# Performance work log

Measured on AMD Instinct MI355X. Metric: run time of the kernel, lower is better.

The kernel has to match this reference:

```python
import jax, jax.numpy as jnp
import numpy as np

# AlphaFold-style Invariant Point Attention (the StructureModule's core op)
N, SD, PD, C, H, PQ, PV = 768, 384, 128, 16, 12, 4, 8
W_C = (2.0 / (9.0 * PQ)) ** 0.5   # point-distance weight
W_L = (1.0 / 3.0) ** 0.5          # logit balancing weight
INV_SQRT_C = C ** -0.5


def setup_inputs() -> dict:
    key = jax.random.key(0)
    ks = jax.random.split(key, 11)
    single_rep = jax.random.normal(ks[0], (N, SD), jnp.float32)
    pair_rep = jax.random.normal(ks[1], (N, N, PD), jnp.float32)
    # random rigid frames: proper orthonormal rotations via QR + translations
    M = jax.random.normal(ks[2], (N, 3, 3), jnp.float32)
    frames_R, _ = jnp.linalg.qr(M)
    frames_t = jax.random.normal(ks[3], (N, 3), jnp.float32) * 10.0
    s = 0.02
    W_qkv = jax.random.normal(ks[4], (SD, 3 * H * C), jnp.float32) * s
    W_b = jax.random.normal(ks[5], (PD, H), jnp.float32) * s
    W_qkp = jax.random.normal(ks[6], (SD, 2 * H * PQ * 3), jnp.float32) * s
    W_vp = jax.random.normal(ks[7], (SD, H * PV * 3), jnp.float32) * s
    gamma = jnp.zeros((H,), jnp.float32)
    W_out = jax.random.normal(ks[8], (H * (PD + C + 3 * PV + PV), SD), jnp.float32) * s
    b_out = jnp.zeros((SD,), jnp.float32)
    return dict(single_rep=single_rep, pair_rep=pair_rep, frames_R=frames_R,
                frames_t=frames_t, W_qkv=W_qkv, W_b=W_b, W_qkp=W_qkp,
                W_vp=W_vp, gamma=gamma, W_out=W_out, b_out=b_out)


def reference(single_rep, pair_rep, frames_R, frames_t,
              W_qkv, W_b, W_qkp, W_vp, gamma, W_out, b_out):
    n = single_rep.shape[0]
    # scalar q/k/v: [n, C, H] (module views as (proj_dim, n_heads))
    q, k, v = [x.reshape(n, C, H) for x in jnp.split(single_rep @ W_qkv, 3, axis=-1)]
    b = jnp.einsum('ijd,dh->ijh', pair_rep, W_b)             # pair bias [n,n,H]
    qp, kp = [x.reshape(n, PQ, 3, H) for x in jnp.split(single_rep @ W_qkp, 2, axis=-1)]
    vp = (single_rep @ W_vp).reshape(n, PV, 3, H)

    def to_global(p):  # apply frame T_i = (R_i, t_i) to local points
        return jnp.einsum('nxy,npyh->npxh', frames_R, p) + frames_t[:, None, :, None]

    qg, kg, vg = to_global(qp), to_global(kp), to_global(vp)

    # squared distances sum_p ||T_i q_p - T_j k_p||^2 without [n,n,PQ,3,H] temp
    sq = jnp.sum(qg * qg, axis=(1, 2))                       # [n,H]
    sk = jnp.sum(kg * kg, axis=(1, 2))                       # [n,H]
    cross = jnp.einsum('ipxh,jpxh->ijh', qg, kg)             # [n,n,H]
    dist2 = sq[:, None, :] + sk[None, :, :] - 2.0 * cross

    head_w = jax.nn.softplus(gamma)                          # per-head gamma
    logits = W_L * (INV_SQRT_C * jnp.einsum('ich,jch->ijh', q, k)
                    + b - 0.5 * W_C * head_w * dist2)
    attn = jax.nn.softmax(logits, axis=1)                    # softmax over j

    o_pair = jnp.einsum('ijh,ijd->ihd', attn, pair_rep)      # [n,H,PD]
    o = jnp.einsum('ijh,jch->ihc', attn, v)                  # [n,H,C]
    og = jnp.einsum('ijh,jpxh->ipxh', attn, vg)              # [n,PV,3,H]
    # back to local frame: R_i^T (og - t_i)
    ol = jnp.einsum('nyx,npyh->npxh', frames_R, og - frames_t[:, None, :, None])
    onorm = jnp.sqrt(jnp.sum(ol * ol, axis=2) + 1e-8)        # [n,PV,H]

    feats = jnp.concatenate([
        o_pair.reshape(n, -1),
        o.reshape(n, -1),
        jnp.moveaxis(ol, -1, 1).reshape(n, -1),
        jnp.moveaxis(onorm, -1, 1).reshape(n, -1)], axis=-1)  # [n, H*(PD+C+3PV+PV)]
    return feats @ W_out + b_out
```

## Files before the change

### kernel.cpp

```cpp
#include <hip/hip_runtime.h>
#include <hip/hip_bf16.h>

typedef float v4f __attribute__((ext_vector_type(4)));
typedef short bf8 __attribute__((ext_vector_type(8)));
typedef unsigned short u16;

constexpr float W_C_ = 0.23570226039551584f;
constexpr float W_L_ = 0.5773502691896258f;

__device__ __forceinline__ u16 f2bf(float f) {
  unsigned u = __float_as_uint(f);
  return (u16)((u + 0x7FFFu + ((u >> 16) & 1u)) >> 16);
}
__device__ __forceinline__ float bf2f(u16 h) {
  return __uint_as_float(((unsigned)h) << 16);
}
__device__ __forceinline__ float dot4(v4f a, v4f b) {
  return a.x * b.x + a.y * b.y + a.z * b.z + a.w * b.w;
}

__global__ __launch_bounds__(256) void convert_bf(const float* __restrict__ src,
                                                  u16* __restrict__ dst, int n8) {
  int idx = blockIdx.x * 256 + threadIdx.x;
  if (idx < n8) {
    v4f a = ((const v4f*)src)[idx * 2];
    v4f b = ((const v4f*)src)[idx * 2 + 1];
    bf8 o;
    o[0] = (short)f2bf(a.x); o[1] = (short)f2bf(a.y);
    o[2] = (short)f2bf(a.z); o[3] = (short)f2bf(a.w);
    o[4] = (short)f2bf(b.x); o[5] = (short)f2bf(b.y);
    o[6] = (short)f2bf(b.z); o[7] = (short)f2bf(b.w);
    ((bf8*)dst)[idx] = o;
  }
}

__global__ __launch_bounds__(256) void wfrag_k(const float* __restrict__ W,
                                               u16* __restrict__ frag,
                                               int K, int N) {
  __shared__ float Ws[32 * 384];
  const int ks = blockIdx.x, k0 = ks * 32, t = threadIdx.x;
  const int NTfull = (N + 15) >> 4;
  for (int n0 = 0; n0 < N; n0 += 384) {
    int PN = N - n0; if (PN > 384) PN = 384;
    __syncthreads();
    for (int idx = t; idx < 32 * PN; idx += 256) {
      int r = idx / PN, c = idx - r * PN;
      Ws[r * PN + c] = W[(size_t)(k0 + r) * N + n0 + c];
    }
    __syncthreads();
    int NTp = (PN + 15) >> 4;
    for (int c = t; c < NTp * 64; c += 256) {
      int nt = c >> 6, l = c & 63;
      int col = nt * 16 + (l & 15);
      bf8 o;
#pragma unroll
      for (int e = 0; e < 8; e++) {
        int rr = (l >> 4) * 8 + e;
        float f = (col < PN) ? Ws[rr * PN + col] : 0.f;
        o[e] = (short)f2bf(f);
      }
      ((bf8*)frag)[((size_t)ks * NTfull + (n0 >> 4) + nt) * 64 + l] = o;
    }
  }
}

__global__ __launch_bounds__(256) void gemm_f32(
    const float* __restrict__ A, const float* __restrict__ B,
    float* __restrict__ C, int M, int N, int K) {
  __shared__ float AsT[32][68];
  __shared__ float Bs[32][36];
  const int bi = blockIdx.y * 64, bj = blockIdx.x * 32;
  const int t = threadIdx.x, ty = t >> 4, tx = t & 15;
  v4f acc0 = {0.f, 0.f, 0.f, 0.f}, acc1 = {0.f, 0.f, 0.f, 0.f};
  for (int k0 = 0; k0 < K; k0 += 32) {
#pragma unroll
    for (int q = 0; q < 2; q++) {
      int idx = t + 256 * q;
      int row = idx >> 3, c4 = idx & 7;
      v4f av = *(const v4f*)(A + (size_t)(bi + row) * K + k0 + c4 * 4);
      AsT[c4 * 4 + 0][row] = av.x;
      AsT[c4 * 4 + 1][row] = av.y;
      AsT[c4 * 4 + 2][row] = av.z;
      AsT[c4 * 4 + 3][row] = av.w;
    }
    {
      int r = t >> 3, c4 = t & 7;
      *(v4f*)&Bs[r][c4 * 4] = *(const v4f*)(B + (size_t)(k0 + r) * N + bj + c4 * 4);
    }
    __syncthreads();
#pragma unroll
    for (int kk = 0; kk < 32; kk++) {
      v4f a = *(const v4f*)&AsT[kk][ty * 4];
      float b0 = Bs[kk][tx * 2], b1 = Bs[kk][tx * 2 + 1];
      acc0 += a * b0;
      acc1 += a * b1;
    }
    __syncthreads();
  }
#pragma unroll
  for (int e = 0; e < 4; e++) {
    int row = bi + ty * 4 + e;
    C[(size_t)row * N + bj + tx * 2] = acc0[e];
    C[(size_t)row * N + bj + tx * 2 + 1] = acc1[e];
  }
}

__global__ __launch_bounds__(256) void mfma_gemm(
    const u16* __restrict__ Abf, const u16* __restrict__ Bfrag,
    const float* __restrict__ bias, float* __restrict__ C,
    int M, int N, int K, int ldc) {
  __shared__ u16 As[64 * 32];
  const int t = threadIdx.x, w = t >> 6, l = t & 63;
  const int bi = blockIdx.y * 64, nt0 = blockIdx.x * 2;
  const int NT = N >> 4, KS = K >> 5;
  v4f acc0 = {0.f, 0.f, 0.f, 0.f}, acc1 = {0.f, 0.f, 0.f, 0.f};
  const int srow = t >> 2, sc = t & 3;
  const int wslot = (sc ^ (srow & 3)) * 8;
  const bf8* Bf = (const bf8*)Bfrag;

  bf8 areg = *(const bf8*)(Abf + (size_t)(bi + srow) * K + sc * 8);
  bf8 b0 = Bf[(size_t)(0 * NT + nt0) * 64 + l];
  bf8 b1 = Bf[(size_t)(0 * NT + nt0 + 1) * 64 + l];
  const int rdoff = (w * 16 + (l & 15)) * 32 + (((l >> 4) ^ (l & 3)) * 8);
  for (int ks = 0; ks < KS; ks++) {
    *(bf8*)&As[srow * 32 + wslot] = areg;
    bf8 an, bn0, bn1;
    if (ks + 1 < KS) {
      an = *(const bf8*)(Abf + (size_t)(bi + srow) * K + (ks + 1) * 32 + sc * 8);
      bn0 = Bf[(size_t)((ks + 1) * NT + nt0) * 64 + l];
      bn1 = Bf[(size_t)((ks + 1) * NT + nt0 + 1) * 64 + l];
    }
    __syncthreads();
    bf8 af = *(const bf8*)&As[rdoff];
    acc0 = __builtin_amdgcn_mfma_f32_16x16x32_bf16(af, b0, acc0, 0, 0, 0);
    acc1 = __builtin_amdgcn_mfma_f32_16x16x32_bf16(af, b1, acc1, 0, 0, 0);
    __syncthreads();
    areg = an; b0 = bn0; b1 = bn1;
  }
  int col0 = nt0 * 16 + (l & 15), col1 = col0 + 16;
  float bb0 = bias ? bias[col0] : 0.f;
  float bb1 = bias ? bias[col1] : 0.f;
#pragma unroll
  for (int r = 0; r < 4; r++) {
    int row = bi + w * 16 + (l >> 4) * 4 + r;
    C[(size_t)row * ldc + col0] = acc0[r] + bb0;
    C[(size_t)row * ldc + col1] = acc1[r] + bb1;
  }
}

__global__ __launch_bounds__(256) void prep_kernel(
    const float* __restrict__ projQKV, const float* __restrict__ projQKP,
    const float* __restrict__ projVP, const float* __restrict__ fR,
    const float* __restrict__ ft,
    float* __restrict__ qbuf, float* __restrict__ v2buf,
    float* __restrict__ qgbuf, float* __restrict__ sqbuf,
    float* __restrict__ kTT) {
  const int n = blockIdx.x, t = threadIdx.x;
  __shared__ float R[9], tt[3];
  __shared__ float qgL[144], kgL[144];
  if (t < 9) R[t] = fR[n * 9 + t];
  if (t < 3) tt[t] = ft[n * 3 + t];
  __syncthreads();
  const float* rQKV = projQKV + (size_t)n * 576;
  const float* rQKP = projQKP + (size_t)n * 288;
  const float* rVP = projVP + (size_t)n * 288;
  if (t < 192) {
    int h = t >> 4, c = t & 15;
    qbuf[(size_t)n * 192 + t] = rQKV[c * 12 + h];
    kTT[(size_t)(h * 29 + c) * 768 + n] = rQKV[192 + c * 12 + h];
    v2buf[(size_t)n * 480 + h * 40 + c] = rQKV[384 + c * 12 + h];
  }
  if (t < 144) {
    int e = t / 12, h = t % 12;
    int p = e / 3, x = e % 3;
    float aq = tt[x], ak = tt[x];
#pragma unroll
    for (int y = 0; y < 3; y++) {
      float r = R[x * 3 + y];
      aq += r * rQKP[p * 36 + y * 12 + h];
      ak += r * rQKP[144 + p * 36 + y * 12 + h];
    }
    qgL[h * 12 + e] = aq;
    kgL[h * 12 + e] = ak;
    qgbuf[(size_t)n * 144 + h * 12 + e] = aq;
    kTT[(size_t)(h * 29 + 16 + e) * 768 + n] = ak;
  }
  for (int idx = t; idx < 288; idx += 256) {
    int e = idx / 12, h = idx % 12;
    int p = e / 3, x = e % 3;
    float a = tt[x];
#pragma unroll
    for (int y = 0; y < 3; y++) a += R[x * 3 + y] * rVP[p * 36 + y * 12 + h];
    v2buf[(size_t)n * 480 + h * 40 + 16 + e] = a;
  }
  __syncthreads();
  if (t < 12) {
    float s = 0.f;
#pragma unroll
    for (int e = 0; e < 12; e++) { float v = qgL[t * 12 + e]; s += v * v; }
    sqbuf[n * 12 + t] = s;
  } else if (t < 24) {
    int h = t - 12;
    float s = 0.f;
#pragma unroll
    for (int e = 0; e < 12; e++) { float v = kgL[h * 12 + e]; s += v * v; }
    kTT[(size_t)(h * 29 + 28) * 768 + n] = s;
  }
}

__global__ __launch_bounds__(256) void bias_mfma(
    const float* __restrict__ pair, const u16* __restrict__ WbFrag,
    u16* __restrict__ bbuf) {
  const int jt = blockIdx.x, i = blockIdx.y;
  const int t = threadIdx.x, w = t >> 6, l = t & 63;
  __shared__ u16 pS[64 * 128];
  bf8 bf[4];
  const bf8* Wf = (const bf8*)WbFrag;
#pragma unroll
  for (int ks = 0; ks < 4; ks++) bf[ks] = Wf[ks * 64 + l];
  const float* pg = pair + ((size_t)i * 768 + jt * 64) * 128;
#pragma unroll
  for (int it = 0; it < 4; it++) {
    int idx = t + 256 * it;
    int j = idx >> 4, c = idx & 15;
    v4f x0 = *(const v4f*)(pg + j * 128 + c * 8);
    v4f x1 = *(const v4f*)(pg + j * 128 + c * 8 + 4);
    bf8 pk;
    pk[0] = (short)f2bf(x0.x); pk[1] = (short)f2bf(x0.y);
    pk[2] = (short)f2bf(x0.z); pk[3] = (short)f2bf(x0.w);
    pk[4] = (short)f2bf(x1.x); pk[5] = (short)f2bf(x1.y);
    pk[6] = (short)f2bf(x1.z); pk[7] = (short)f2bf(x1.w);
    *(bf8*)&pS[j * 128 + ((c ^ (j & 15)) * 8)] = pk;
  }
  __syncthreads();
  v4f acc = {0.f, 0.f, 0.f, 0.f};
#pragma unroll
  for (int ks = 0; ks < 4; ks++) {
    int slot = (ks * 4 + (l >> 4)) ^ (l & 15);
    bf8 af = *(const bf8*)&pS[(w * 16 + (l & 15)) * 128 + slot * 8];
    acc = __builtin_amdgcn_mfma_f32_16x16x32_bf16(af, bf[ks], acc, 0, 0, 0);
  }
  int h = l & 15;
  if (h < 12) {
    int jbase = jt * 64 + w * 16 + (l >> 4) * 4;
    u16* dst = bbuf + ((size_t)i * 12 + h) * 768 + jbase;
#pragma unroll
    for (int r = 0; r < 4; r++) dst[r] = f2bf(acc[r]);
  }
}

__global__ __launch_bounds__(256) void qk_softmax(
    const float* __restrict__ qbuf, const float* __restrict__ qgbuf,
    const float* __restrict__ sqbuf, const float* __restrict__ kTT,
    const u16* __restrict__ bbuf, const float* __restrict__ gamma,
    u16* __restrict__ attn) {
  const int h = blockIdx.x, i = blockIdx.y, t = threadIdx.x;
  __shared__ float red[8];
  float q[16], qg[12];
  const float* qb = qbuf + (size_t)i * 192 + h * 16;
  const float* qgb = qgbuf + (size_t)i * 144 + h * 12;
#pragma unroll
  for (int c = 0; c < 16; c++) q[c] = qb[c];
#pragma unroll
  for (int e = 0; e < 12; e++) qg[e] = qgb[e];
  float sq = sqbuf[i * 12 + h];
  float g = gamma[h];
  float hw = fmaxf(g, 0.f) + log1pf(expf(-fabsf(g)));
  const float* kb = kTT + (size_t)h * 29 * 768;
  const u16* brow = bbuf + ((size_t)i * 12 + h) * 768;
  float lg[3];
#pragma unroll
  for (int s = 0; s < 3; s++) {
    int j = t + 256 * s;
    float qk = 0.f;
#pragma unroll
    for (int c = 0; c < 16; c++) qk += q[c] * kb[c * 768 + j];
    float cr = 0.f;
#pragma unroll
    for (int e = 0; e < 12; e++) cr += qg[e] * kb[(16 + e) * 768 + j];
    float sk = kb[28 * 768 + j];
    float b = bf2f(brow[j]);
    float d2 = sq + sk - 2.f * cr;
    lg[s] = W_L_ * (0.25f * qk + b - 0.5f * W_C_ * hw * d2);
  }
  float m = fmaxf(fmaxf(lg[0], lg[1]), lg[2]);
#pragma unroll
  for (int o = 32; o >= 1; o >>= 1) m = fmaxf(m, __shfl_xor(m, o));
  if ((t & 63) == 0) red[t >> 6] = m;
  __syncthreads();
  m = fmaxf(fmaxf(red[0], red[1]), fmaxf(red[2], red[3]));
  float p0 = __expf(lg[0] - m), p1 = __expf(lg[1] - m), p2 = __expf(lg[2] - m);
  float ss = p0 + p1 + p2;
#pragma unroll
  for (int o = 32; o >= 1; o >>= 1) ss += __shfl_xor(ss, o);
  if ((t & 63) == 0) red[4 + (t >> 6)] = ss;
  __syncthreads();
  float inv = 1.f / (red[4] + red[5] + red[6] + red[7]);
  u16* arow = attn + ((size_t)i * 12 + h) * 768;
  arow[t] = f2bf(p0 * inv);
  arow[t + 256] = f2bf(p1 * inv);
  arow[t + 512] = f2bf(p2 * inv);
}

__global__ __launch_bounds__(256) void opair_k(
    const float* __restrict__ pair, const u16* __restrict__ attn,
    u16* __restrict__ feats_bf) {
  const int i = blockIdx.x, t = threadIdx.x;
  const int w = t >> 6, l = t & 63;
  const int dq = l & 31, hh = l >> 5;
  __shared__ float pairL[64][132];
  __shared__ float ALf[12][68];
  v4f acc[6];
#pragma unroll
  for (int k = 0; k < 6; k++) acc[k] = (v4f){0.f, 0.f, 0.f, 0.f};

  v4f pr[8];
  bf8 areg;
  {
    const float* pg = pair + ((size_t)i * 768) * 128;
#pragma unroll
    for (int it = 0; it < 8; it++) {
      int idx = t + 256 * it;
      pr[it] = *(const v4f*)(pg + (idx >> 5) * 128 + (idx & 31) * 4);
    }
    if (t < 96)
      areg = *(const bf8*)(attn + ((size_t)i * 12 + (t >> 3)) * 768 + (t & 7) * 8);
  }
  for (int jt = 0; jt < 12; jt++) {
#pragma unroll
    for (int it = 0; it < 8; it++) {
      int idx = t + 256 * it;
      *(v4f*)&pairL[idx >> 5][(idx & 31) * 4] = pr[it];
    }
    if (t < 96) {
      int hA = t >> 3, c = t & 7;
#pragma unroll
      for (int e = 0; e < 8; e++) ALf[hA][c * 8 + e] = bf2f((u16)areg[e]);
    }
    if (jt < 11) {
      const float* pg = pair + ((size_t)i * 768 + (jt + 1) * 64) * 128;
#pragma unroll
      for (int it = 0; it < 8; it++) {
        int idx = t + 256 * it;
        pr[it] = *(const v4f*)(pg + (idx >> 5) * 128 + (idx & 31) * 4);
      }
      if (t < 96)
        areg = *(const bf8*)(attn + ((size_t)i * 12 + (t >> 3)) * 768 +
                             (jt + 1) * 64 + (t & 7) * 8);
    }
    __syncthreads();
#pragma unroll
    for (int jj16 = 0; jj16 < 16; jj16++) {
      int jj = w * 16 + jj16;
      v4f pv = *(const v4f*)&pairL[jj][dq * 4];
      float a0 = ALf[hh * 6 + 0][jj];
      float a1 = ALf[hh * 6 + 1][jj];
      float a2 = ALf[hh * 6 + 2][jj];
      float a3 = ALf[hh * 6 + 3][jj];
      float a4 = ALf[hh * 6 + 4][jj];
      float a5 = ALf[hh * 6 + 5][jj];
      acc[0] += pv * a0; acc[1] += pv * a1; acc[2] += pv * a2;
      acc[3] += pv * a3; acc[4] += pv * a4; acc[5] += pv * a5;
    }
    __syncthreads();
  }
  float* red = &pairL[0][0];
#pragma unroll
  for (int k = 0; k < 6; k++)
    *(v4f*)&red[((w * 12 + hh * 6 + k) << 7) + dq * 4] = acc[k];
  __syncthreads();
  const size_t fb = (size_t)i * 2112;
#pragma unroll
  for (int s = 0; s < 6; s++) {
    int o = t + 256 * s;
    int ho = o >> 7, dd = o & 127;
    float v = red[(ho << 7) + dd] + red[((12 + ho) << 7) + dd] +
              red[((24 + ho) << 7) + dd] + red[((36 + ho) << 7) + dd];
    feats_bf[fb + o] = f2bf(v);
  }
}

__global__ __launch_bounds__(256) void ov_k(
    const u16* __restrict__ attn, const float* __restrict__ v2buf,
    float* __restrict__ O2) {
  const int i0 = blockIdx.x * 64, h = blockIdx.y, t = threadIdx.x;
  __shared__ float AL[64][65];
  __shared__ float VL[64][48];
  const int il = t & 63, eb = (t >> 6) * 12;
  v4f acc0 = {0.f, 0.f, 0.f, 0.f}, acc1 = {0.f, 0.f, 0.f, 0.f},
      acc2 = {0.f, 0.f, 0.f, 0.f};
  for (int jt = 0; jt < 12; ++jt) {
    const int j0 = jt * 64;
#pragma unroll
    for (int q = 0; q < 2; q++) {
      int idx = t + 256 * q;
      int ii = idx >> 3, c = idx & 7;
      bf8 av = *(const bf8*)(attn + ((size_t)(i0 + ii) * 12 + h) * 768 + j0 + c * 8);
#pragma unroll
      for (int e = 0; e < 8; e++) AL[ii][c * 8 + e] = bf2f((u16)av[e]);
    }
#pragma unroll
    for (int q = 0; q < 3; q++) {
      int idx = t + q * 256;
      if (idx < 640) {
        int jj = idx / 10, e4 = idx % 10;
        *(v4f*)&VL[jj][e4 * 4] =
            *(const v4f*)(v2buf + (size_t)(j0 + jj) * 480 + h * 40 + e4 * 4);
      }
    }
    __syncthreads();
#pragma unroll 4
    for (int jj = 0; jj < 64; ++jj) {
      float a = AL[il][jj];
      v4f v0 = *(const v4f*)&VL[jj][eb];
      v4f v1 = *(const v4f*)&VL[jj][eb + 4];
      v4f v2 = *(const v4f*)&VL[jj][eb + 8];
      acc0 += v0 * a;
      acc1 += v1 * a;
      acc2 += v2 * a;
    }
    __syncthreads();
  }
  float* orow = O2 + ((size_t)(i0 + il) * 12 + h) * 40;
#pragma unroll
  for (int s = 0; s < 12; ++s) {
    int e = eb + s;
    if (e < 40) {
      float v = (s < 4) ? ((float*)&acc0)[s]
                        : (s < 8) ? ((float*)&acc1)[s - 4] : ((float*)&acc2)[s - 8];
      orow[e] = v;
    }
  }
}

__global__ __launch_bounds__(256) void finalize_k(
    const float* __restrict__ O2, const float* __restrict__ fR,
    const float* __restrict__ ft, u16* __restrict__ feats_bf) {
  const int i = blockIdx.x, t = threadIdx.x;
  __shared__ float RL[9], ttL[3];
  if (t < 9) RL[t] = fR[i * 9 + t];
  if (t < 3) ttL[t] = ft[i * 3 + t];
  __syncthreads();
  const float* orow = O2 + (size_t)i * 480;
  const size_t fb = (size_t)i * 2112;
  if (t < 192) {
    int h = t >> 4, c = t & 15;
    feats_bf[fb + 1536 + h * 16 + c] = f2bf(orow[h * 40 + c]);
  }
  if (t < 96) {
    int h = t >> 3, p = t & 7;
    float og0 = orow[h * 40 + 16 + p * 3 + 0] - ttL[0];
    float og1 = orow[h * 40 + 16 + p * 3 + 1] - ttL[1];
    float og2 = orow[h * 40 + 16 + p * 3 + 2] - ttL[2];
    float o0 = RL[0] * og0 + RL[3] * og1 + RL[6] * og2;
    float o1 = RL[1] * og0 + RL[4] * og1 + RL[7] * og2;
    float o2 = RL[2] * og0 + RL[5] * og1 + RL[8] * og2;
    feats_bf[fb + 1728 + h * 24 + p * 3 + 0] = f2bf(o0);
    feats_bf[fb + 1728 + h * 24 + p * 3 + 1] = f2bf(o1);
    feats_bf[fb + 1728 + h * 24 + p * 3 + 2] = f2bf(o2);
    feats_bf[fb + 2016 + h * 8 + p] = f2bf(sqrtf(o0 * o0 + o1 * o1 + o2 * o2 + 1e-8f));
  }
}

extern "C" void kernel_launch(void* const* d_in, const int* in_sizes, int n_in,
                              void* d_out, int out_size, void* d_ws, size_t ws_size,
                              hipStream_t stream) {
  const float* single = (const float*)d_in[0];
  const float* pair = (const float*)d_in[1];
  const float* fR = (const float*)d_in[2];
  const float* ft = (const float*)d_in[3];
  const float* W_qkv = (const float*)d_in[4];
  const float* W_b = (const float*)d_in[5];
  const float* W_qkp = (const float*)d_in[6];
  const float* W_vp = (const float*)d_in[7];
  const float* gamma = (const float*)d_in[8];
  const float* W_out = (const float*)d_in[9];
  const float* b_out = (const float*)d_in[10];
  float* out = (float*)d_out;

  float* ws = (float*)d_ws;
  float* projQKV = ws;
  float* projQKP = projQKV + 442368;
  float* projVP  = projQKP + 221184;
  float* qbuf    = projVP + 221184;
  float* v2buf   = qbuf + 147456;
  float* qgbuf   = v2buf + 368640;
  float* sqbuf   = qgbuf + 110592;
  float* kTT     = sqbuf + 9216;
  float* O2      = kTT + 267264;
  u16* single_bf = (u16*)(O2 + 368640);
  u16* WqkvFrag  = single_bf + 294912;
  u16* WbFrag    = WqkvFrag + 221184;
  u16* WoutFrag  = WbFrag + 2048;
  u16* bbuf      = WoutFrag + 811008;
  u16* attn      = bbuf + 7077888;
  u16* feats_bf  = attn + 7077888;

  convert_bf<<<144, 256, 0, stream>>>(single, single_bf, 36864);
  wfrag_k<<<12, 256, 0, stream>>>(W_qkv, WqkvFrag, 384, 576);
  wfrag_k<<<4, 256, 0, stream>>>(W_b, WbFrag, 128, 12);
  wfrag_k<<<66, 256, 0, stream>>>(W_out, WoutFrag, 2112, 384);
  gemm_f32<<<dim3(9, 12), 256, 0, stream>>>(single, W_qkp, projQKP, 768, 288, 384);
  gemm_f32<<<dim3(9, 12), 256, 0, stream>>>(single, W_vp, projVP, 768, 288, 384);
  mfma_gemm<<<dim3(18, 12), 256, 0, stream>>>(single_bf, WqkvFrag, nullptr,
                                              projQKV, 768, 576, 384, 576);
  prep_kernel<<<768, 256, 0, stream>>>(projQKV, projQKP, projVP, fR, ft,
                                       qbuf, v2buf, qgbuf, sqbuf, kTT);
  bias_mfma<<<dim3(12, 768), 256, 0, stream>>>(pair, WbFrag, bbuf);
  qk_softmax<<<dim3(12, 768), 256, 0, stream>>>(qbuf, qgbuf, sqbuf, kTT, bbuf,
                                                gamma, attn);
  opair_k<<<768, 256, 0, stream>>>(pair, attn, feats_bf);
  ov_k<<<dim3(12, 12), 256, 0, stream>>>(attn, v2buf, O2);
  finalize_k<<<768, 256, 0, stream>>>(O2, fR, ft, feats_bf);
  mfma_gemm<<<dim3(12, 12), 256, 0, stream>>>(feats_bf, WoutFrag, b_out,
                                              out, 768, 384, 2112, 384);
}
```

Before: 310.6 us.

## Fuse pair bias, logits, online softmax and pair aggregation into one kernel

Replaces the separate bias_mfma, qk_softmax and opair_k kernels with a fused flash-style kernel. Each block handles one row i and one quarter of j, computes the bias with MFMA, adds the scalar and point logits, runs an online softmax, and accumulates the attention-weighted pair features while the pair tile is still in shared memory. A small reduce kernel then merges the four partial results. This means pair_rep (the dominant tensor) is read once instead of twice, and the bias and attn round trips through global memory go away. In exchange it keeps per-tile unnormalized probabilities plus max values so that ov_k can rescale them, which adds partial buffers and extra exp work.

```diff
diff --git a/kernel.cpp b/kernel.cpp
--- a/kernel.cpp
+++ b/kernel.cpp
@@ -36,7 +36,7 @@
 
 __global__ __launch_bounds__(256) void wfrag_k(const float* __restrict__ W,
                                                u16* __restrict__ frag,
-                                               int K, int N) {
+                                               int K, int N, float scale) {
   __shared__ float Ws[32 * 384];
   const int ks = blockIdx.x, k0 = ks * 32, t = threadIdx.x;
   const int NTfull = (N + 15) >> 4;
@@ -56,7 +56,7 @@
 #pragma unroll
       for (int e = 0; e < 8; e++) {
         int rr = (l >> 4) * 8 + e;
-        float f = (col < PN) ? Ws[rr * PN + col] : 0.f;
+        float f = (col < PN) ? Ws[rr * PN + col] * scale : 0.f;
         o[e] = (short)f2bf(f);
       }
       ((bf8*)frag)[((size_t)ks * NTfull + (n0 >> 4) + nt) * 64 + l] = o;
@@ -152,9 +152,9 @@
     const float* __restrict__ projQKV, const float* __restrict__ projQKP,
     const float* __restrict__ projVP, const float* __restrict__ fR,
     const float* __restrict__ ft,
-    float* __restrict__ qbuf, float* __restrict__ v2buf,
-    float* __restrict__ qgbuf, float* __restrict__ sqbuf,
-    float* __restrict__ kTT) {
+    float* __restrict__ qbuf, float* __restrict__ kbuf, float* __restrict__ v2buf,
+    float* __restrict__ qgbuf, float* __restrict__ kgbuf,
+    float* __restrict__ sqbuf, float* __restrict__ skbuf) {
   const int n = blockIdx.x, t = threadIdx.x;
   __shared__ float R[9], tt[3];
   __shared__ float qgL[144], kgL[144];
@@ -167,7 +167,7 @@
   if (t < 192) {
     int h = t >> 4, c = t & 15;
     qbuf[(size_t)n * 192 + t] = rQKV[c * 12 + h];
-    kTT[(size_t)(h * 29 + c) * 768 + n] = rQKV[192 + c * 12 + h];
+    kbuf[(size_t)n * 192 + t] = rQKV[192 + c * 12 + h];
     v2buf[(size_t)n * 480 + h * 40 + c] = rQKV[384 + c * 12 + h];
   }
   if (t < 144) {
@@ -183,7 +183,7 @@
     qgL[h * 12 + e] = aq;
     kgL[h * 12 + e] = ak;
     qgbuf[(size_t)n * 144 + h * 12 + e] = aq;
-    kTT[(size_t)(h * 29 + 16 + e) * 768 + n] = ak;
+    kgbuf[(size_t)n * 144 + h * 12 + e] = ak;
   }
   for (int idx = t; idx < 288; idx += 256) {
     int e = idx / 12, h = idx % 12;
@@ -204,185 +204,232 @@
     float s = 0.f;
 #pragma unroll
     for (int e = 0; e < 12; e++) { float v = kgL[h * 12 + e]; s += v * v; }
-    kTT[(size_t)(h * 29 + 28) * 768 + n] = s;
-  }
-}
-
-__global__ __launch_bounds__(256) void bias_mfma(
+    skbuf[n * 12 + h] = s;
+  }
+}
+
+__global__ __launch_bounds__(256) void ipa_fused(
     const float* __restrict__ pair, const u16* __restrict__ WbFrag,
-    u16* __restrict__ bbuf) {
-  const int jt = blockIdx.x, i = blockIdx.y;
-  const int t = threadIdx.x, w = t >> 6, l = t & 63;
+    const float* __restrict__ gamma,
+    const float* __restrict__ qbuf, const float* __restrict__ kbuf,
+    const float* __restrict__ qgbuf, const float* __restrict__ kgbuf,
+    const float* __restrict__ sqbuf, const float* __restrict__ skbuf,
+    u16* __restrict__ pW, float* __restrict__ mTW,
+    float* __restrict__ opP, float* __restrict__ mlP) {
+  const int ch = blockIdx.x, i = blockIdx.y, t = threadIdx.x;
+  const int w = t >> 6, l = t & 63;
   __shared__ u16 pS[64 * 128];
-  bf8 bf[4];
+  __shared__ float lgL[64 * 14];
+  __shared__ float pL[64 * 12];
+  __shared__ float qL[192], qgL[144];
+  __shared__ float c1L[12], c2L[12], mL[12], lL[12], rL[12];
+
+  if (t < 192) qL[t] = qbuf[(size_t)i * 192 + t];
+  if (t < 144) qgL[t] = qgbuf[(size_t)i * 144 + t];
+  if (t < 12) {
+    float g = gamma[t];
+    float hw = fmaxf(g, 0.f) + log1pf(expf(-fabsf(g)));
+    c1L[t] = W_L_ * W_C_ * hw;
+    c2L[t] = -0.5f * c1L[t] * sqbuf[i * 12 + t];
+    mL[t] = -1e30f;
+    lL[t] = 0.f;
+  }
+  bf8 wb[4];
   const bf8* Wf = (const bf8*)WbFrag;
 #pragma unroll
-  for (int ks = 0; ks < 4; ks++) bf[ks] = Wf[ks * 64 + l];
-  const float* pg = pair + ((size_t)i * 768 + jt * 64) * 128;
-#pragma unroll
-  for (int it = 0; it < 4; it++) {
-    int idx = t + 256 * it;
-    int j = idx >> 4, c = idx & 15;
-    v4f x0 = *(const v4f*)(pg + j * 128 + c * 8);
-    v4f x1 = *(const v4f*)(pg + j * 128 + c * 8 + 4);
-    bf8 pk;
-    pk[0] = (short)f2bf(x0.x); pk[1] = (short)f2bf(x0.y);
-    pk[2] = (short)f2bf(x0.z); pk[3] = (short)f2bf(x0.w);
-    pk[4] = (short)f2bf(x1.x); pk[5] = (short)f2bf(x1.y);
-    pk[6] = (short)f2bf(x1.z); pk[7] = (short)f2bf(x1.w);
-    *(bf8*)&pS[j * 128 + ((c ^ (j & 15)) * 8)] = pk;
-  }
+  for (int ks = 0; ks < 4; ks++) wb[ks] = Wf[ks * 64 + l];
+
+  v4f pr[8];
+  {
+    const float* pg = pair + ((size_t)i * 768 + ch * 192) * 128;
+#pragma unroll
+    for (int it = 0; it < 4; it++) {
+      int idx = t + 256 * it;
+      int j = idx >> 4, c = idx & 15;
+      pr[2 * it] = *(const v4f*)(pg + j * 128 + c * 8);
+      pr[2 * it + 1] = *(const v4f*)(pg + j * 128 + c * 8 + 4);
+    }
+  }
+  float opacc[6];
+#pragma unroll
+  for (int k = 0; k < 6; k++) opacc[k] = 0.f;
+  const int d = t & 127, hb6 = (t >> 7) * 6;
+  const bool lohalf = (t < 128);
   __syncthreads();
-  v4f acc = {0.f, 0.f, 0.f, 0.f};
-#pragma unroll
-  for (int ks = 0; ks < 4; ks++) {
-    int slot = (ks * 4 + (l >> 4)) ^ (l & 15);
-    bf8 af = *(const bf8*)&pS[(w * 16 + (l & 15)) * 128 + slot * 8];
-    acc = __builtin_amdgcn_mfma_f32_16x16x32_bf16(af, bf[ks], acc, 0, 0, 0);
-  }
-  int h = l & 15;
-  if (h < 12) {
-    int jbase = jt * 64 + w * 16 + (l >> 4) * 4;
-    u16* dst = bbuf + ((size_t)i * 12 + h) * 768 + jbase;
-#pragma unroll
-    for (int r = 0; r < 4; r++) dst[r] = f2bf(acc[r]);
-  }
-}
-
-__global__ __launch_bounds__(256) void qk_softmax(
-    const float* __restrict__ qbuf, const float* __restrict__ qgbuf,
-    const float* __restrict__ sqbuf, const float* __restrict__ kTT,
-    const u16* __restrict__ bbuf, const float* __restrict__ gamma,
-    u16* __restrict__ attn) {
-  const int h = blockIdx.x, i = blockIdx.y, t = threadIdx.x;
-  __shared__ float red[8];
-  float q[16], qg[12];
-  const float* qb = qbuf + (size_t)i * 192 + h * 16;
-  const float* qgb = qgbuf + (size_t)i * 144 + h * 12;
-#pragma unroll
-  for (int c = 0; c < 16; c++) q[c] = qb[c];
-#pragma unroll
-  for (int e = 0; e < 12; e++) qg[e] = qgb[e];
-  float sq = sqbuf[i * 12 + h];
-  float g = gamma[h];
-  float hw = fmaxf(g, 0.f) + log1pf(expf(-fabsf(g)));
-  const float* kb = kTT + (size_t)h * 29 * 768;
-  const u16* brow = bbuf + ((size_t)i * 12 + h) * 768;
-  float lg[3];
-#pragma unroll
-  for (int s = 0; s < 3; s++) {
-    int j = t + 256 * s;
-    float qk = 0.f;
-#pragma unroll
-    for (int c = 0; c < 16; c++) qk += q[c] * kb[c * 768 + j];
-    float cr = 0.f;
-#pragma unroll
-    for (int e = 0; e < 12; e++) cr += qg[e] * kb[(16 + e) * 768 + j];
-    float sk = kb[28 * 768 + j];
-    float b = bf2f(brow[j]);
-    float d2 = sq + sk - 2.f * cr;
-    lg[s] = W_L_ * (0.25f * qk + b - 0.5f * W_C_ * hw * d2);
-  }
-  float m = fmaxf(fmaxf(lg[0], lg[1]), lg[2]);
-#pragma unroll
-  for (int o = 32; o >= 1; o >>= 1) m = fmaxf(m, __shfl_xor(m, o));
-  if ((t & 63) == 0) red[t >> 6] = m;
-  __syncthreads();
-  m = fmaxf(fmaxf(red[0], red[1]), fmaxf(red[2], red[3]));
-  float p0 = __expf(lg[0] - m), p1 = __expf(lg[1] - m), p2 = __expf(lg[2] - m);
-  float ss = p0 + p1 + p2;
-#pragma unroll
-  for (int o = 32; o >= 1; o >>= 1) ss += __shfl_xor(ss, o);
-  if ((t & 63) == 0) red[4 + (t >> 6)] = ss;
-  __syncthreads();
-  float inv = 1.f / (red[4] + red[5] + red[6] + red[7]);
-  u16* arow = attn + ((size_t)i * 12 + h) * 768;
-  arow[t] = f2bf(p0 * inv);
-  arow[t + 256] = f2bf(p1 * inv);
-  arow[t + 512] = f2bf(p2 * inv);
-}
-
-__global__ __launch_bounds__(256) void opair_k(
-    const float* __restrict__ pair, const u16* __restrict__ attn,
+
+  for (int tile = 0; tile < 3; tile++) {
+    const int jg0 = ch * 192 + tile * 64;
+#pragma unroll
+    for (int it = 0; it < 4; it++) {
+      int idx = t + 256 * it;
+      int j = idx >> 4, c = idx & 15;
+      v4f x0 = pr[2 * it], x1 = pr[2 * it + 1];
+      bf8 pk;
+      pk[0] = (short)f2bf(x0.x); pk[1] = (short)f2bf(x0.y);
+      pk[2] = (short)f2bf(x0.z); pk[3] = (short)f2bf(x0.w);
+      pk[4] = (short)f2bf(x1.x); pk[5] = (short)f2bf(x1.y);
+      pk[6] = (short)f2bf(x1.z); pk[7] = (short)f2bf(x1.w);
+      *(bf8*)&pS[j * 128 + ((c ^ (j & 15)) * 8)] = pk;
+    }
+    if (tile < 2) {
+      const float* pg = pair + ((size_t)i * 768 + jg0 + 64) * 128;
+#pragma unroll
+      for (int it = 0; it < 4; it++) {
+        int idx = t + 256 * it;
+        int j = idx >> 4, c = idx & 15;
+        pr[2 * it] = *(const v4f*)(pg + j * 128 + c * 8);
+        pr[2 * it + 1] = *(const v4f*)(pg + j * 128 + c * 8 + 4);
+      }
+    }
+    __syncthreads();
+    {
+      v4f acc = {0.f, 0.f, 0.f, 0.f};
+#pragma unroll
+      for (int ks = 0; ks < 4; ks++) {
+        int slot = (ks * 4 + (l >> 4)) ^ (l & 15);
+        bf8 af = *(const bf8*)&pS[(w * 16 + (l & 15)) * 128 + slot * 8];
+        acc = __builtin_amdgcn_mfma_f32_16x16x32_bf16(af, wb[ks], acc, 0, 0, 0);
+      }
+      int h = l & 15;
+      if (h < 12) {
+#pragma unroll
+        for (int r = 0; r < 4; r++)
+          lgL[(w * 16 + (l >> 4) * 4 + r) * 14 + h] = acc[r];
+      }
+    }
+    __syncthreads();
+    {
+      const int j = t >> 2, hg = t & 3;
+      const int jg = jg0 + j;
+#pragma unroll
+      for (int hh = 0; hh < 3; hh++) {
+        int h = hg * 3 + hh;
+        const v4f* kk = (const v4f*)(kbuf + (size_t)jg * 192 + h * 16);
+        const v4f* qq = (const v4f*)&qL[h * 16];
+        float qk = dot4(kk[0], qq[0]) + dot4(kk[1], qq[1]) +
+                   dot4(kk[2], qq[2]) + dot4(kk[3], qq[3]);
+        const v4f* kg = (const v4f*)(kgbuf + (size_t)jg * 144 + h * 12);
+        const v4f* qg = (const v4f*)&qgL[h * 12];
+        float cr = dot4(kg[0], qg[0]) + dot4(kg[1], qg[1]) + dot4(kg[2], qg[2]);
+        float sk = skbuf[(size_t)jg * 12 + h];
+        lgL[j * 14 + h] += 0.25f * W_L_ * qk + c1L[h] * (cr - 0.5f * sk) + c2L[h];
+      }
+    }
+    __syncthreads();
+    if (t < 192) {
+      const int h = t >> 4, jj = t & 15;
+      float lg0 = lgL[(jj * 4 + 0) * 14 + h];
+      float lg1 = lgL[(jj * 4 + 1) * 14 + h];
+      float lg2 = lgL[(jj * 4 + 2) * 14 + h];
+      float lg3 = lgL[(jj * 4 + 3) * 14 + h];
+      float tmax = fmaxf(fmaxf(lg0, lg1), fmaxf(lg2, lg3));
+#pragma unroll
+      for (int m = 1; m < 16; m <<= 1) tmax = fmaxf(tmax, __shfl_xor(tmax, m));
+      float p0 = __expf(lg0 - tmax), p1 = __expf(lg1 - tmax);
+      float p2 = __expf(lg2 - tmax), p3 = __expf(lg3 - tmax);
+      {
+        u16* dst = pW + ((size_t)i * 12 + h) * 768 + jg0 + jj * 4;
+        unsigned lo = (unsigned)f2bf(p0) | ((unsigned)f2bf(p1) << 16);
+        unsigned hi = (unsigned)f2bf(p2) | ((unsigned)f2bf(p3) << 16);
+        uint2 pk2; pk2.x = lo; pk2.y = hi;
+        *(uint2*)dst = pk2;
+      }
+      float mold = mL[h];
+      float mnew = fmaxf(mold, tmax);
+      float st = __expf(tmax - mnew);
+      float rr = __expf(mold - mnew);
+      pL[(jj * 4 + 0) * 12 + h] = p0 * st;
+      pL[(jj * 4 + 1) * 12 + h] = p1 * st;
+      pL[(jj * 4 + 2) * 12 + h] = p2 * st;
+      pL[(jj * 4 + 3) * 12 + h] = p3 * st;
+      float ps = (p0 + p1 + p2 + p3) * st;
+#pragma unroll
+      for (int m = 1; m < 16; m <<= 1) ps += __shfl_xor(ps, m);
+      if (jj == 0) {
+        mTW[((size_t)i * 12 + h) * 12 + ch * 3 + tile] = tmax;
+        rL[h] = rr;
+        lL[h] = lL[h] * rr + ps;
+        mL[h] = mnew;
+      }
+    }
+    __syncthreads();
+    {
+#pragma unroll
+      for (int k = 0; k < 6; k++) opacc[k] *= rL[hb6 + k];
+      const int dtop = d >> 3, dlow = d & 7;
+#pragma unroll 4
+      for (int jj = 0; jj < 64; jj++) {
+        float pv = bf2f(pS[jj * 128 + ((dtop ^ (jj & 15)) << 3) + dlow]);
+        const v4f* pp = (const v4f*)&pL[jj * 12];
+        v4f pm = pp[1];
+        if (lohalf) {
+          v4f pa = pp[0];
+          opacc[0] += pa.x * pv; opacc[1] += pa.y * pv;
+          opacc[2] += pa.z * pv; opacc[3] += pa.w * pv;
+          opacc[4] += pm.x * pv; opacc[5] += pm.y * pv;
+        } else {
+          v4f pc = pp[2];
+          opacc[0] += pm.z * pv; opacc[1] += pm.w * pv;
+          opacc[2] += pc.x * pv; opacc[3] += pc.y * pv;
+          opacc[4] += pc.z * pv; opacc[5] += pc.w * pv;
+        }
+      }
+    }
+    __syncthreads();
+  }
+#pragma unroll
+  for (int k = 0; k < 6; k++)
+    opP[((size_t)(i * 4 + ch) * 12 + hb6 + k) * 128 + d] = opacc[k];
+  if (t < 12) {
+    mlP[(size_t)(i * 4 + ch) * 24 + t] = mL[t];
+    mlP[(size_t)(i * 4 + ch) * 24 + 12 + t] = lL[t];
+  }
+}
+
+__global__ __launch_bounds__(256) void reduce_k(
+    const float* __restrict__ opP, const float* __restrict__ mlP,
+    float* __restrict__ Mg, float* __restrict__ iDg,
     u16* __restrict__ feats_bf) {
   const int i = blockIdx.x, t = threadIdx.x;
-  const int w = t >> 6, l = t & 63;
-  const int dq = l & 31, hh = l >> 5;
-  __shared__ float pairL[64][132];
-  __shared__ float ALf[12][68];
-  v4f acc[6];
-#pragma unroll
-  for (int k = 0; k < 6; k++) acc[k] = (v4f){0.f, 0.f, 0.f, 0.f};
-
-  v4f pr[8];
-  bf8 areg;
-  {
-    const float* pg = pair + ((size_t)i * 768) * 128;
-#pragma unroll
-    for (int it = 0; it < 8; it++) {
-      int idx = t + 256 * it;
-      pr[it] = *(const v4f*)(pg + (idx >> 5) * 128 + (idx & 31) * 4);
-    }
-    if (t < 96)
-      areg = *(const bf8*)(attn + ((size_t)i * 12 + (t >> 3)) * 768 + (t & 7) * 8);
-  }
-  for (int jt = 0; jt < 12; jt++) {
-#pragma unroll
-    for (int it = 0; it < 8; it++) {
-      int idx = t + 256 * it;
-      *(v4f*)&pairL[idx >> 5][(idx & 31) * 4] = pr[it];
-    }
-    if (t < 96) {
-      int hA = t >> 3, c = t & 7;
-#pragma unroll
-      for (int e = 0; e < 8; e++) ALf[hA][c * 8 + e] = bf2f((u16)areg[e]);
-    }
-    if (jt < 11) {
-      const float* pg = pair + ((size_t)i * 768 + (jt + 1) * 64) * 128;
-#pragma unroll
-      for (int it = 0; it < 8; it++) {
-        int idx = t + 256 * it;
-        pr[it] = *(const v4f*)(pg + (idx >> 5) * 128 + (idx & 31) * 4);
-      }
-      if (t < 96)
-        areg = *(const bf8*)(attn + ((size_t)i * 12 + (t >> 3)) * 768 +
-                             (jt + 1) * 64 + (t & 7) * 8);
-    }
-    __syncthreads();
-#pragma unroll
-    for (int jj16 = 0; jj16 < 16; jj16++) {
-      int jj = w * 16 + jj16;
-      v4f pv = *(const v4f*)&pairL[jj][dq * 4];
-      float a0 = ALf[hh * 6 + 0][jj];
-      float a1 = ALf[hh * 6 + 1][jj];
-      float a2 = ALf[hh * 6 + 2][jj];
-      float a3 = ALf[hh * 6 + 3][jj];
-      float a4 = ALf[hh * 6 + 4][jj];
-      float a5 = ALf[hh * 6 + 5][jj];
-      acc[0] += pv * a0; acc[1] += pv * a1; acc[2] += pv * a2;
-      acc[3] += pv * a3; acc[4] += pv * a4; acc[5] += pv * a5;
-    }
-    __syncthreads();
-  }
-  float* red = &pairL[0][0];
-#pragma unroll
-  for (int k = 0; k < 6; k++)
-    *(v4f*)&red[((w * 12 + hh * 6 + k) << 7) + dq * 4] = acc[k];
+  __shared__ float wcL[4][12], invDL[12];
+  if (t < 12) {
+    float mc[4], lc[4];
+#pragma unroll
+    for (int c = 0; c < 4; c++) {
+      mc[c] = mlP[(size_t)(i * 4 + c) * 24 + t];
+      lc[c] = mlP[(size_t)(i * 4 + c) * 24 + 12 + t];
+    }
+    float M = fmaxf(fmaxf(mc[0], mc[1]), fmaxf(mc[2], mc[3]));
+    float D = 0.f;
+#pragma unroll
+    for (int c = 0; c < 4; c++) {
+      float wv = __expf(mc[c] - M);
+      wcL[c][t] = wv;
+      D += lc[c] * wv;
+    }
+    float iD = 1.f / D;
+    invDL[t] = iD;
+    Mg[i * 12 + t] = M;
+    iDg[i * 12 + t] = iD;
+  }
   __syncthreads();
   const size_t fb = (size_t)i * 2112;
 #pragma unroll
   for (int s = 0; s < 6; s++) {
     int o = t + 256 * s;
-    int ho = o >> 7, dd = o & 127;
-    float v = red[(ho << 7) + dd] + red[((12 + ho) << 7) + dd] +
-              red[((24 + ho) << 7) + dd] + red[((36 + ho) << 7) + dd];
-    feats_bf[fb + o] = f2bf(v);
+    int h = o >> 7, dd = o & 127;
+    float v = 0.f;
+#pragma unroll
+    for (int c = 0; c < 4; c++)
+      v += opP[((size_t)(i * 4 + c) * 12 + h) * 128 + dd] * wcL[c][h];
+    feats_bf[fb + o] = f2bf(v * invDL[h]);
   }
 }
 
 __global__ __launch_bounds__(256) void ov_k(
-    const u16* __restrict__ attn, const float* __restrict__ v2buf,
-    float* __restrict__ O2) {
+    const u16* __restrict__ pW, const float* __restrict__ mTW,
+    const float* __restrict__ Mg, const float* __restrict__ iDg,
+    const float* __restrict__ v2buf, float* __restrict__ O2) {
   const int i0 = blockIdx.x * 64, h = blockIdx.y, t = threadIdx.x;
   __shared__ float AL[64][65];
   __shared__ float VL[64][48];
@@ -395,9 +442,12 @@
     for (int q = 0; q < 2; q++) {
       int idx = t + 256 * q;
       int ii = idx >> 3, c = idx & 7;
-      bf8 av = *(const bf8*)(attn + ((size_t)(i0 + ii) * 12 + h) * 768 + j0 + c * 8);
-#pragma unroll
-      for (int e = 0; e < 8; e++) AL[ii][c * 8 + e] = bf2f((u16)av[e]);
+      int ig = i0 + ii;
+      float sc = __expf(mTW[((size_t)ig * 12 + h) * 12 + jt] - Mg[ig * 12 + h]) *
+                 iDg[ig * 12 + h];
+      bf8 av = *(const bf8*)(pW + ((size_t)ig * 12 + h) * 768 + j0 + c * 8);
+#pragma unroll
+      for (int e = 0; e < 8; e++) AL[ii][c * 8 + e] = bf2f((u16)av[e]) * sc;
     }
 #pragma unroll
     for (int q = 0; q < 3; q++) {
@@ -480,37 +530,44 @@
 
   float* ws = (float*)d_ws;
   float* projQKV = ws;
-  float* projQKP = projQKV + 442368;
-  float* projVP  = projQKP + 221184;
-  float* qbuf    = projVP + 221184;
-  float* v2buf   = qbuf + 147456;
-  float* qgbuf   = v2buf + 368640;
-  float* sqbuf   = qgbuf + 110592;
-  float* kTT     = sqbuf + 9216;
-  float* O2      = kTT + 267264;
-  u16* single_bf = (u16*)(O2 + 368640);
-  u16* WqkvFrag  = single_bf + 294912;
-  u16* WbFrag    = WqkvFrag + 221184;
-  u16* WoutFrag  = WbFrag + 2048;
-  u16* bbuf      = WoutFrag + 811008;
-  u16* attn      = bbuf + 7077888;
-  u16* feats_bf  = attn + 7077888;
+  float* projQKP = ws + 442368;
+  float* projVP  = ws + 663552;
+  float* qbuf    = ws + 884736;
+  float* kbuf    = ws + 1032192;
+  float* v2buf   = ws + 1179648;
+  float* qgbuf   = ws + 1548288;
+  float* kgbuf   = ws + 1658880;
+  float* sqbuf   = ws + 1769472;
+  float* skbuf   = ws + 1778688;
+  float* opP     = ws + 1787904;
+  float* mlP     = ws + 6506496;
+  float* mTW     = ws + 6580224;
+  float* Mg      = ws + 6690816;
+  float* iDg     = ws + 6700032;
+  float* O2      = ws + 6709248;
+  u16* ub        = (u16*)(ws + 7077888);
+  u16* single_bf = ub;
+  u16* WqkvFrag  = ub + 294912;
+  u16* WbFrag    = ub + 516096;
+  u16* WoutFrag  = ub + 518144;
+  u16* pW        = ub + 1329152;
+  u16* feats_bf  = ub + 8407040;
 
   convert_bf<<<144, 256, 0, stream>>>(single, single_bf, 36864);
-  wfrag_k<<<12, 256, 0, stream>>>(W_qkv, WqkvFrag, 384, 576);
-  wfrag_k<<<4, 256, 0, stream>>>(W_b, WbFrag, 128, 12);
-  wfrag_k<<<66, 256, 0, stream>>>(W_out, WoutFrag, 2112, 384);
+  wfrag_k<<<12, 256, 0, stream>>>(W_qkv, WqkvFrag, 384, 576, 1.f);
+  wfrag_k<<<4, 256, 0, stream>>>(W_b, WbFrag, 128, 12, W_L_);
+  wfrag_k<<<66, 256, 0, stream>>>(W_out, WoutFrag, 2112, 384, 1.f);
   gemm_f32<<<dim3(9, 12), 256, 0, stream>>>(single, W_qkp, projQKP, 768, 288, 384);
   gemm_f32<<<dim3(9, 12), 256, 0, stream>>>(single, W_vp, projVP, 768, 288, 384);
   mfma_gemm<<<dim3(18, 12), 256, 0, stream>>>(single_bf, WqkvFrag, nullptr,
                                               projQKV, 768, 576, 384, 576);
   prep_kernel<<<768, 256, 0, stream>>>(projQKV, projQKP, projVP, fR, ft,
-                                       qbuf, v2buf, qgbuf, sqbuf, kTT);
-  bias_mfma<<<dim3(12, 768), 256, 0, stream>>>(pair, WbFrag, bbuf);
-  qk_softmax<<<dim3(12, 768), 256, 0, stream>>>(qbuf, qgbuf, sqbuf, kTT, bbuf,
-                                                gamma, attn);
-  opair_k<<<768, 256, 0, stream>>>(pair, attn, feats_bf);
-  ov_k<<<dim3(12, 12), 256, 0, stream>>>(attn, v2buf, O2);
+                                       qbuf, kbuf, v2buf, qgbuf, kgbuf, sqbuf, skbuf);
+  ipa_fused<<<dim3(4, 768), 256, 0, stream>>>(pair, WbFrag, gamma, qbuf, kbuf,
+                                              qgbuf, kgbuf, sqbuf, skbuf,
+                                              pW, mTW, opP, mlP);
+  reduce_k<<<768, 256, 0, stream>>>(opP, mlP, Mg, iDg, feats_bf);
+  ov_k<<<dim3(12, 12), 256, 0, stream>>>(pW, mTW, Mg, iDg, v2buf, O2);
   finalize_k<<<768, 256, 0, stream>>>(O2, fR, ft, feats_bf);
   mfma_gemm<<<dim3(12, 12), 256, 0, stream>>>(feats_bf, WoutFrag, b_out,
                                               out, 768, 384, 2112, 384);
```

New measurement: 391.3 us. 1.26x slower.
